# Optimization experiments

Measured on AMD Instinct MI355X. Metric: run time of the kernel, lower is better.

The kernel has to match this reference:

```python
import jax, jax.numpy as jnp
import numpy as np

N = 8192      # number of nodes
D = 16        # inp_dim (forced by W: [16,18])
DH = 18       # GAT hidden dim (forced by W/a)
H = 8         # num_heads


def setup_inputs() -> dict:
    key = jax.random.key(0)
    k1, k2, k3, k4 = jax.random.split(key, 4)
    inputs = jax.random.normal(k1, (N, D), dtype=jnp.float32)
    # xavier-ish init scale for W (torch uses xavier_uniform gain=1.414)
    W = jax.random.normal(k2, (D, DH), dtype=jnp.float32) * np.float32(np.sqrt(2.0 / (D + DH)) * 1.414)
    a = jax.random.normal(k3, (2 * DH, 1), dtype=jnp.float32) * np.float32(0.1)
    Wk = jax.random.normal(k4, (H, D, D), dtype=jnp.float32)  # stacked attention_wts_k
    return {"inputs": inputs, "W": W, "a": a, "Wk": Wk}


def reference(inputs, W, a, Wk):
    # h = inputs @ W  -> [N, 18]
    h = jnp.matmul(inputs, W)
    # a_input[i, j] = concat(h[i], h[j]); score e[i,j] = a_input[i,j] @ a.
    # Decompose instead of materializing [N*N, 36]:
    #   e[i,j] = h[i] @ a[:18] + h[j] @ a[18:]
    a1 = a[:DH, 0]  # [18]
    a2 = a[DH:, 0]  # [18]
    e = (h @ a1)[:, None] + (h @ a2)[None, :]        # [N, N]
    # softmax over dim=-2 of [N, N, 1] == axis 1 of [N, N] (neighbor axis)
    score = jax.nn.softmax(e, axis=1)                # [N, N]
    # per-head linear: op1[h] = inputs @ Wk[h]  -> [H, N, 16]
    op1 = jnp.einsum('nd,hde->hne', inputs, Wk)
    # scored_x sum over neighbors: out[i,h,:] = sum_j score[i,j] * op1[h,j,:]
    out = jnp.einsum('nm,hmd->nhd', score, op1)      # [N, H, 16]
    return out.reshape(N, H * D)                     # concat heads -> [N, 128]
```

## Files before the change

### kernel.cpp

```cpp
#include <hip/hip_runtime.h>
#include <hip/hip_bf16.h>

#define N 8192
#define D 16
#define DH 18
#define H 8
#define NBLK_A 32

typedef float v4f __attribute__((ext_vector_type(4)));


__global__ void attn_partial(const float* __restrict__ x, const float* __restrict__ W,
                             const float* __restrict__ a, float* __restrict__ ws) {
    __shared__ float w2[D];
    __shared__ float part[4][D + 1];
    int t = threadIdx.x;
    if (t < D) {
        float acc = 0.f;
        #pragma unroll
        for (int j = 0; j < DH; ++j) acc += W[t * DH + j] * a[DH + j];
        w2[t] = acc;
    }
    __syncthreads();

    int m = blockIdx.x * blockDim.x + t;
    const float4* xp = reinterpret_cast<const float4*>(x + (size_t)m * D);
    float4 q0 = xp[0], q1 = xp[1], q2 = xp[2], q3 = xp[3];
    float xv[D];
    xv[0]=q0.x; xv[1]=q0.y; xv[2]=q0.z; xv[3]=q0.w;
    xv[4]=q1.x; xv[5]=q1.y; xv[6]=q1.z; xv[7]=q1.w;
    xv[8]=q2.x; xv[9]=q2.y; xv[10]=q2.z; xv[11]=q2.w;
    xv[12]=q3.x; xv[13]=q3.y; xv[14]=q3.z; xv[15]=q3.w;

    float g = 0.f;
    #pragma unroll
    for (int d = 0; d < D; ++d) g += xv[d] * w2[d];
    float w = expf(g);

    float acc[D + 1];
    acc[0] = w;
    #pragma unroll
    for (int d = 0; d < D; ++d) acc[1 + d] = w * xv[d];

    #pragma unroll
    for (int off = 32; off > 0; off >>= 1) {
        #pragma unroll
        for (int k = 0; k < D + 1; ++k)
            acc[k] += __shfl_down(acc[k], off, 64);
    }
    int wave = t >> 6, lane = t & 63;
    if (lane == 0) {
        #pragma unroll
        for (int k = 0; k < D + 1; ++k) part[wave][k] = acc[k];
    }
    __syncthreads();
    if (t < D + 1) {
        float s = part[0][t] + part[1][t] + part[2][t] + part[3][t];
        ws[t * NBLK_A + blockIdx.x] = s;
    }
}

__global__ void attn_write(const float* __restrict__ Wk, const float* __restrict__ ws,
                           float* __restrict__ out) {
    __shared__ float sv[D + 1];
    __shared__ float ov[H * D];
    int t = threadIdx.x;
    if (t < D + 1) {
        float s = 0.f;
        #pragma unroll
        for (int b = 0; b < NBLK_A; ++b) s += ws[t * NBLK_A + b];
        sv[t] = s;
    }
    __syncthreads();
    if (t < H * D) {
        int h = t >> 4, e = t & 15;
        float inv = 1.0f / sv[0];
        float acc = 0.f;
        #pragma unroll
        for (int d = 0; d < D; ++d)
            acc += sv[1 + d] * Wk[h * (D * D) + d * D + e];
        ov[t] = acc * inv;
    }
    __syncthreads();

    const v4f* ov4 = reinterpret_cast<const v4f*>(ov);
    v4f* out4 = reinterpret_cast<v4f*>(out);
    const v4f val = ov4[t & 31];
    const int total = N * (H * D / 4);
    for (int idx = blockIdx.x * blockDim.x + t; idx < total; idx += gridDim.x * blockDim.x) {
        __builtin_nontemporal_store(val, &out4[idx]);
    }
}

extern "C" void kernel_launch(void* const* d_in, const int* in_sizes, int n_in,
                              void* d_out, int out_size, void* d_ws, size_t ws_size,
                              hipStream_t stream) {
    const float* inputs = (const float*)d_in[0];
    const float* W      = (const float*)d_in[1];
    const float* a      = (const float*)d_in[2];
    const float* Wk     = (const float*)d_in[3];
    float* out = (float*)d_out;
    float* ws  = (float*)d_ws;

    attn_partial<<<NBLK_A, 256, 0, stream>>>(inputs, W, a, ws);
    attn_write<<<256, 256, 0, stream>>>(Wk, ws, out);
}
```

Before: 64.80 us.

## Fuse reduction and broadcast write into one kernel with redundant per-block reduction

Replaces the two-kernel pipeline (partial reductions into workspace, then a combine plus broadcast write) with one kernel. Every block redundantly reduces all N rows of the input to get the softmax-weighted sums, then writes its own 1024-vector slice of the output. This removes a kernel launch and the workspace round trip, at the cost of 256× redundant reads of the 512KB input, which should mostly hit in L2. The code before already relies on the softmax weights not depending on the row index i, so the output is identical across rows.

```diff
diff --git a/kernel.cpp b/kernel.cpp
--- a/kernel.cpp
+++ b/kernel.cpp
@@ -1,46 +1,61 @@
 #include <hip/hip_runtime.h>
-#include <hip/hip_bf16.h>
 
 #define N 8192
 #define D 16
 #define DH 18
 #define H 8
-#define NBLK_A 32
 
 typedef float v4f __attribute__((ext_vector_type(4)));
 
-
-__global__ void attn_partial(const float* __restrict__ x, const float* __restrict__ W,
-                             const float* __restrict__ a, float* __restrict__ ws) {
+__global__ __launch_bounds__(256) void attn_fused(
+        const float* __restrict__ x, const float* __restrict__ W,
+        const float* __restrict__ a, const float* __restrict__ Wk,
+        float* __restrict__ out) {
     __shared__ float w2[D];
     __shared__ float part[4][D + 1];
-    int t = threadIdx.x;
+    __shared__ float sv[D + 1];
+    __shared__ float ov[H * D];
+    const int t = threadIdx.x;
+
     if (t < D) {
-        float acc = 0.f;
+        float s = 0.f;
         #pragma unroll
-        for (int j = 0; j < DH; ++j) acc += W[t * DH + j] * a[DH + j];
-        w2[t] = acc;
+        for (int j = 0; j < DH; ++j) s += W[t * DH + j] * a[DH + j];
+        w2[t] = s;
     }
     __syncthreads();
 
-    int m = blockIdx.x * blockDim.x + t;
-    const float4* xp = reinterpret_cast<const float4*>(x + (size_t)m * D);
-    float4 q0 = xp[0], q1 = xp[1], q2 = xp[2], q3 = xp[3];
-    float xv[D];
-    xv[0]=q0.x; xv[1]=q0.y; xv[2]=q0.z; xv[3]=q0.w;
-    xv[4]=q1.x; xv[5]=q1.y; xv[6]=q1.z; xv[7]=q1.w;
-    xv[8]=q2.x; xv[9]=q2.y; xv[10]=q2.z; xv[11]=q2.w;
-    xv[12]=q3.x; xv[13]=q3.y; xv[14]=q3.z; xv[15]=q3.w;
-
-    float g = 0.f;
+    float w2r[D];
     #pragma unroll
-    for (int d = 0; d < D; ++d) g += xv[d] * w2[d];
-    float w = expf(g);
+    for (int d = 0; d < D; ++d) w2r[d] = w2[d];
 
     float acc[D + 1];
-    acc[0] = w;
     #pragma unroll
-    for (int d = 0; d < D; ++d) acc[1 + d] = w * xv[d];
+    for (int k = 0; k < D + 1; ++k) acc[k] = 0.f;
+
+    const v4f* xp = reinterpret_cast<const v4f*>(x);
+    #pragma unroll 4
+    for (int r = 0; r < N / 256; ++r) {
+        const int m = r * 256 + t;
+        v4f q0 = xp[m * 4 + 0];
+        v4f q1 = xp[m * 4 + 1];
+        v4f q2 = xp[m * 4 + 2];
+        v4f q3 = xp[m * 4 + 3];
+        float xv[D];
+        xv[0]=q0.x;  xv[1]=q0.y;  xv[2]=q0.z;  xv[3]=q0.w;
+        xv[4]=q1.x;  xv[5]=q1.y;  xv[6]=q1.z;  xv[7]=q1.w;
+        xv[8]=q2.x;  xv[9]=q2.y;  xv[10]=q2.z; xv[11]=q2.w;
+        xv[12]=q3.x; xv[13]=q3.y; xv[14]=q3.z; xv[15]=q3.w;
+
+        float g = 0.f;
+        #pragma unroll
+        for (int d = 0; d < D; ++d) g += xv[d] * w2r[d];
+        const float w = expf(g);
+
+        acc[0] += w;
+        #pragma unroll
+        for (int d = 0; d < D; ++d) acc[1 + d] += w * xv[d];
+    }
 
     #pragma unroll
     for (int off = 32; off > 0; off >>= 1) {
@@ -48,48 +63,34 @@
         for (int k = 0; k < D + 1; ++k)
             acc[k] += __shfl_down(acc[k], off, 64);
     }
-    int wave = t >> 6, lane = t & 63;
+    const int wave = t >> 6, lane = t & 63;
     if (lane == 0) {
         #pragma unroll
         for (int k = 0; k < D + 1; ++k) part[wave][k] = acc[k];
     }
     __syncthreads();
-    if (t < D + 1) {
-        float s = part[0][t] + part[1][t] + part[2][t] + part[3][t];
-        ws[t * NBLK_A + blockIdx.x] = s;
-    }
-}
+    if (t < D + 1)
+        sv[t] = part[0][t] + part[1][t] + part[2][t] + part[3][t];
+    __syncthreads();
 
-__global__ void attn_write(const float* __restrict__ Wk, const float* __restrict__ ws,
-                           float* __restrict__ out) {
-    __shared__ float sv[D + 1];
-    __shared__ float ov[H * D];
-    int t = threadIdx.x;
-    if (t < D + 1) {
+    if (t < H * D) {
+        const int h = t >> 4, e = t & 15;
+        const float inv = 1.0f / sv[0];
         float s = 0.f;
         #pragma unroll
-        for (int b = 0; b < NBLK_A; ++b) s += ws[t * NBLK_A + b];
-        sv[t] = s;
-    }
-    __syncthreads();
-    if (t < H * D) {
-        int h = t >> 4, e = t & 15;
-        float inv = 1.0f / sv[0];
-        float acc = 0.f;
-        #pragma unroll
         for (int d = 0; d < D; ++d)
-            acc += sv[1 + d] * Wk[h * (D * D) + d * D + e];
-        ov[t] = acc * inv;
+            s += sv[1 + d] * Wk[h * (D * D) + d * D + e];
+        ov[t] = s * inv;
     }
     __syncthreads();
 
     const v4f* ov4 = reinterpret_cast<const v4f*>(ov);
     v4f* out4 = reinterpret_cast<v4f*>(out);
     const v4f val = ov4[t & 31];
-    const int total = N * (H * D / 4);
-    for (int idx = blockIdx.x * blockDim.x + t; idx < total; idx += gridDim.x * blockDim.x) {
-        __builtin_nontemporal_store(val, &out4[idx]);
-    }
+    const int base = blockIdx.x * 1024 + t;
+    #pragma unroll
+    for (int i = 0; i < 4; ++i)
+        __builtin_nontemporal_store(val, &out4[base + i * 256]);
 }
 
 extern "C" void kernel_launch(void* const* d_in, const int* in_sizes, int n_in,
@@ -100,8 +101,6 @@
     const float* a      = (const float*)d_in[2];
     const float* Wk     = (const float*)d_in[3];
     float* out = (float*)d_out;
-    float* ws  = (float*)d_ws;
 
-    attn_partial<<<NBLK_A, 256, 0, stream>>>(inputs, W, a, ws);
-    attn_write<<<256, 256, 0, stream>>>(Wk, ws, out);
+    attn_fused<<<256, 256, 0, stream>>>(inputs, W, a, Wk, out);
 }
```

Result: slower. 72.56 us (+12.0%).
